# Performance work log

Measured on AMD Instinct MI355X. Metric: run time of the kernel, lower is better.

The kernel has to match this reference:

```python
import jax, jax.numpy as jnp
import numpy as np

NODE_DIM = 256
EDGE_DIM = 64
NUM_HEADS = 8
HEAD_DIM = NODE_DIM // NUM_HEADS
B, N = 2, 512


def setup_inputs() -> dict:
    key = jax.random.key(0)
    ks = jax.random.split(key, 16)
    s_n = 1.0 / np.sqrt(NODE_DIM)
    s_e = 1.0 / np.sqrt(EDGE_DIM)
    inp = {
        "node_tensors": jax.random.normal(ks[0], (B, N, NODE_DIM), jnp.float32),
        "edge_tensors": jax.random.normal(ks[1], (B, N, N, EDGE_DIM), jnp.float32),
        # nn.Linear params: W is [out, in], y = x @ W.T + b
        "Wnq": jax.random.uniform(ks[2], (NODE_DIM, NODE_DIM), jnp.float32, -s_n, s_n),
        "bnq": jax.random.uniform(ks[3], (NODE_DIM,), jnp.float32, -s_n, s_n),
        "Wnk": jax.random.uniform(ks[4], (NODE_DIM, NODE_DIM), jnp.float32, -s_n, s_n),
        "bnk": jax.random.uniform(ks[5], (NODE_DIM,), jnp.float32, -s_n, s_n),
        "Wnv": jax.random.uniform(ks[6], (NODE_DIM, NODE_DIM), jnp.float32, -s_n, s_n),
        "bnv": jax.random.uniform(ks[7], (NODE_DIM,), jnp.float32, -s_n, s_n),
        "Weq": jax.random.uniform(ks[8], (NODE_DIM, EDGE_DIM), jnp.float32, -s_e, s_e),
        "beq": jax.random.uniform(ks[9], (NODE_DIM,), jnp.float32, -s_e, s_e),
        "Wek": jax.random.uniform(ks[10], (NODE_DIM, EDGE_DIM), jnp.float32, -s_e, s_e),
        "bek": jax.random.uniform(ks[11], (NODE_DIM,), jnp.float32, -s_e, s_e),
        "Wev": jax.random.uniform(ks[12], (NODE_DIM, EDGE_DIM), jnp.float32, -s_e, s_e),
        "bev": jax.random.uniform(ks[13], (NODE_DIM,), jnp.float32, -s_e, s_e),
    }
    return inp


def _node_heads(x):
    # [B, N, node_dim] -> [B, H, N, Dh]
    b, n, _ = x.shape
    return x.reshape(b, n, NUM_HEADS, HEAD_DIM).transpose(0, 2, 1, 3)


def _edge_heads(x):
    # [B, N, N, node_dim] -> [B, H, N, N, Dh]
    b, n, m, _ = x.shape
    return x.reshape(b, n, m, NUM_HEADS, HEAD_DIM).transpose(0, 3, 1, 2, 4)


def reference(node_tensors, edge_tensors, Wnq, bnq, Wnk, bnk, Wnv, bnv,
              Weq, beq, Wek, bek, Wev, bev):
    scale = 1.0 / np.sqrt(HEAD_DIM)
    nq = _node_heads(node_tensors @ Wnq.T + bnq)  # [B,H,N,Dh]
    nk = _node_heads(node_tensors @ Wnk.T + bnk)
    nv = _node_heads(node_tensors @ Wnv.T + bnv)
    eq = _edge_heads(edge_tensors @ Weq.T + beq)  # [B,H,N,N,Dh]
    ek = _edge_heads(edge_tensors @ Wek.T + bek)
    ev = _edge_heads(edge_tensors @ Wev.T + bev)
    # qk[b,h,i,j] = sum_d (eq[bhijd] + nq[bhid]) * (ek[bhijd] + nk[bhjd])
    qk = (jnp.einsum('bhijd,bhijd->bhij', eq, ek)
          + jnp.einsum('bhijd,bhjd->bhij', eq, nk)
          + jnp.einsum('bhid,bhijd->bhij', nq, ek)
          + jnp.einsum('bhid,bhjd->bhij', nq, nk))
    att = jax.nn.softmax(qk * scale, axis=-1)  # [B,H,N,N]
    # out[b,h,i,d] = sum_j att[bhij] * (ev[bhijd] + nv[bhjd])
    out = (jnp.einsum('bhij,bhijd->bhid', att, ev)
           + jnp.einsum('bhij,bhjd->bhid', att, nv))
    b, h, n, d = out.shape
    return out.transpose(0, 2, 1, 3).reshape(b, n, NODE_DIM)
```

## Files before the change

### kernel.cpp

```cpp
#include <hip/hip_runtime.h>

typedef __bf16 bf16x8 __attribute__((ext_vector_type(8)));
typedef float  f32x4  __attribute__((ext_vector_type(4)));
typedef unsigned int u32x4 __attribute__((ext_vector_type(4)));

#define B_   2
#define N_   512
#define ND_  256
#define ED_  64
#define NH_  8
#define DH_  32

static __device__ __forceinline__ unsigned pack_bf16(float a, float b) {
    unsigned short ua = __builtin_bit_cast(unsigned short, (__bf16)a);
    unsigned short ub = __builtin_bit_cast(unsigned short, (__bf16)b);
    return (unsigned)ua | ((unsigned)ub << 16);
}

__global__ __launch_bounds__(256) void cvt_w_kernel(
    const float* __restrict__ wq, const float* __restrict__ wk,
    const float* __restrict__ wv, unsigned short* __restrict__ w16)
{
    int id = blockIdx.x * 256 + threadIdx.x;
    const float* src = (id < 16384) ? wq : (id < 32768 ? wk : wv);
    int idx = id & 16383;
    w16[id] = __builtin_bit_cast(unsigned short, (__bf16)src[idx]);
}

__global__ __launch_bounds__(256) void trans_w_kernel(
    const float* __restrict__ Wq, const float* __restrict__ Wk,
    const float* __restrict__ Wv, float* __restrict__ Wt)
{
    __shared__ float t[32][33];
    const int bx = blockIdx.x;
    const int m  = bx >> 6;
    const int t6 = bx & 63;
    const int cb = (t6 >> 3) << 5;
    const int kb = (t6 & 7) << 5;
    const float* W = (m == 0) ? Wq : (m == 1 ? Wk : Wv);
    const int tx = threadIdx.x & 31, ty = threadIdx.x >> 5;
    #pragma unroll
    for (int s = 0; s < 4; s++)
        t[ty + 8 * s][tx] = W[(size_t)(cb + ty + 8 * s) * ND_ + kb + tx];
    __syncthreads();
    float* dst = Wt + (size_t)m * ND_ * ND_;
    #pragma unroll
    for (int s = 0; s < 4; s++)
        dst[(size_t)(kb + ty + 8 * s) * ND_ + cb + tx] = t[tx][ty + 8 * s];
}

__global__ __launch_bounds__(256) void qkv_kernel(
    const float* __restrict__ node, const float* __restrict__ Wt,
    const float* __restrict__ bnq, const float* __restrict__ bnk,
    const float* __restrict__ bnv, const float* __restrict__ beq,
    const float* __restrict__ bek, const float* __restrict__ bev,
    float* __restrict__ Qh, float* __restrict__ KVp)
{
    __shared__ float xs[4][ND_];
    const int c   = threadIdx.x;
    const int m   = blockIdx.x >> 8;
    const int grp = blockIdx.x & 255;
    const int g0  = grp * 4;
    {
        const int r = c >> 6, col4 = (c & 63) * 4;
        const float4 v = *reinterpret_cast<const float4*>(node + (size_t)(g0 + r) * ND_ + col4);
        *reinterpret_cast<float4*>(&xs[r][col4]) = v;
    }
    __syncthreads();

    const float* Wm = Wt + (size_t)m * ND_ * ND_;
    float acc[4] = {0.f, 0.f, 0.f, 0.f};
    for (int k = 0; k < ND_; k += 4) {
        const float w0 = Wm[(size_t)(k + 0) * ND_ + c];
        const float w1 = Wm[(size_t)(k + 1) * ND_ + c];
        const float w2 = Wm[(size_t)(k + 2) * ND_ + c];
        const float w3 = Wm[(size_t)(k + 3) * ND_ + c];
        #pragma unroll
        for (int rr = 0; rr < 4; rr++) {
            const float4 x = *reinterpret_cast<const float4*>(&xs[rr][k]);
            acc[rr] += x.x * w0 + x.y * w1 + x.z * w2 + x.w * w3;
        }
    }
    const float bias = (m == 0) ? (bnq[c] + beq[c])
                     : (m == 1) ? (bnk[c] + bek[c])
                                : (bnv[c] + bev[c]);
    const int h = c >> 5, d = c & 31;
    #pragma unroll
    for (int rr = 0; rr < 4; rr++) {
        const int g  = g0 + rr;
        const int bb = g >> 9, ii = g & (N_ - 1);
        const int bh = bb * NH_ + h;
        const float y = acc[rr] + bias;
        if (m == 0) {
            Qh[((size_t)bh * N_ + ii) * DH_ + d] = y;
        } else {
            const int set = ((m == 1) ? 0 : 2) + (d >> 4);
            const size_t idx = (((size_t)bh * 32 + (ii >> 4)) * 4 + set) * 256
                             + (size_t)((((d >> 2) & 3) * 16 + (ii & 15)) * 4 + (d & 3));
            KVp[idx] = y;
        }
    }
}

__global__ __launch_bounds__(512, 2) void attn_kernel(
    const float* __restrict__ edge,
    const float* __restrict__ Qh, const float* __restrict__ KVp,
    const unsigned short* __restrict__ W16, float* __restrict__ out)
{
    __shared__ unsigned short lds_[2][2][64 * 72];

    const int tid  = threadIdx.x;
    const int lane = tid & 63;
    const int h    = tid >> 6;
    const int q4   = lane >> 4;
    const int l15  = lane & 15;
    const int blk  = blockIdx.x;
    const int b    = blk >> 8;
    const int i0   = (blk & 255) * 2;
    const int bh   = b * NH_ + h;

    bf16x8 wf[3][2][2];
    #pragma unroll
    for (int m = 0; m < 3; m++)
        #pragma unroll
        for (int hf = 0; hf < 2; hf++)
            #pragma unroll
            for (int ks = 0; ks < 2; ks++) {
                const u32x4* p = reinterpret_cast<const u32x4*>(
                    W16 + m * (ND_ * ED_) + (h * DH_ + hf * 16 + l15) * ED_ + ks * 32 + q4 * 8);
                wf[m][hf][ks] = __builtin_bit_cast(bf16x8, *p);
            }

    f32x4 Cq[2][2];
    {
        const float* Qrow = Qh + ((size_t)bh * N_ + i0) * DH_;
        Cq[0][0] = *reinterpret_cast<const f32x4*>(Qrow + q4 * 4);
        Cq[0][1] = *reinterpret_cast<const f32x4*>(Qrow + 16 + q4 * 4);
        Cq[1][0] = *reinterpret_cast<const f32x4*>(Qrow + DH_ + q4 * 4);
        Cq[1][1] = *reinterpret_cast<const f32x4*>(Qrow + DH_ + 16 + q4 * 4);
    }

    const f32x4* kvb = reinterpret_cast<const f32x4*>(KVp + (size_t)bh * 32 * 1024) + lane;

    const float* eb0 = edge + ((size_t)(b * N_ + i0)) * N_ * ED_;
    const float* eb1 = eb0 + (size_t)N_ * ED_;

    float l_acc[2] = {0.f, 0.f};
    f32x4 o0[2] = {{0.f,0.f,0.f,0.f},{0.f,0.f,0.f,0.f}};
    f32x4 o1[2] = {{0.f,0.f,0.f,0.f},{0.f,0.f,0.f,0.f}};
    const float scale = 0.17677669529663687f;

    float4 g[2][2];
    {
        const float4* e0 = reinterpret_cast<const float4*>(eb0);
        const float4* e1 = reinterpret_cast<const float4*>(eb1);
        g[0][0] = e0[tid]; g[0][1] = e0[tid + 512];
        g[1][0] = e1[tid]; g[1][1] = e1[tid + 512];
    }
    #pragma unroll
    for (int ii = 0; ii < 2; ii++) {
        unsigned short* buf = lds_[0][ii];
        #pragma unroll
        for (int pt = 0; pt < 2; pt++) {
            const float4 gg = g[ii][pt];
            const int f = tid + pt * 512;
            const int row = f >> 4, c4 = f & 15;
            uint2 v = {pack_bf16(gg.x, gg.y), pack_bf16(gg.z, gg.w)};
            *reinterpret_cast<uint2*>(buf + row * 72 + c4 * 4) = v;
        }
    }
    f32x4 kn0 = kvb[0], kn1 = kvb[64], vn0 = kvb[128], vn1 = kvb[192];
    __syncthreads();

    #pragma unroll 1
    for (int ch = 0; ch < 8; ch++) {
        if (ch < 7) {
            const float4* e0 = reinterpret_cast<const float4*>(eb0 + (ch + 1) * 4096);
            const float4* e1 = reinterpret_cast<const float4*>(eb1 + (ch + 1) * 4096);
            g[0][0] = e0[tid]; g[0][1] = e0[tid + 512];
            g[1][0] = e1[tid]; g[1][1] = e1[tid + 512];
        }
        const unsigned short* buf0 = lds_[ch & 1][0];
        const unsigned short* buf1 = lds_[ch & 1][1];

        #pragma unroll 2
        for (int sub = 0; sub < 4; sub++) {
            const int jg = ch * 4 + sub;
            const f32x4 Ck0 = kn0, Ck1 = kn1, Cv0 = vn0, Cv1 = vn1;
            {
                const f32x4* p = kvb + ((jg + 1) & 31) * 256;
                kn0 = p[0]; kn1 = p[64]; vn0 = p[128]; vn1 = p[192];
            }
            const unsigned short* ar0 = buf0 + (sub * 16 + l15) * 72 + q4 * 8;
            const unsigned short* ar1 = buf1 + (sub * 16 + l15) * 72 + q4 * 8;
            const bf16x8 a00 = __builtin_bit_cast(bf16x8, *reinterpret_cast<const u32x4*>(ar0));
            const bf16x8 a01 = __builtin_bit_cast(bf16x8, *reinterpret_cast<const u32x4*>(ar0 + 32));
            const bf16x8 a10 = __builtin_bit_cast(bf16x8, *reinterpret_cast<const u32x4*>(ar1));
            const bf16x8 a11 = __builtin_bit_cast(bf16x8, *reinterpret_cast<const u32x4*>(ar1 + 32));

            #pragma unroll
            for (int ii = 0; ii < 2; ii++) {
                const bf16x8 aA = ii ? a10 : a00;
                const bf16x8 aB = ii ? a11 : a01;
                f32x4 eq0 = __builtin_amdgcn_mfma_f32_16x16x32_bf16(wf[0][0][0], aA, Cq[ii][0], 0, 0, 0);
                f32x4 eq1 = __builtin_amdgcn_mfma_f32_16x16x32_bf16(wf[0][1][0], aA, Cq[ii][1], 0, 0, 0);
                f32x4 ek0 = __builtin_amdgcn_mfma_f32_16x16x32_bf16(wf[1][0][0], aA, Ck0, 0, 0, 0);
                f32x4 ek1 = __builtin_amdgcn_mfma_f32_16x16x32_bf16(wf[1][1][0], aA, Ck1, 0, 0, 0);
                f32x4 ev0 = __builtin_amdgcn_mfma_f32_16x16x32_bf16(wf[2][0][0], aA, Cv0, 0, 0, 0);
                f32x4 ev1 = __builtin_amdgcn_mfma_f32_16x16x32_bf16(wf[2][1][0], aA, Cv1, 0, 0, 0);
                eq0 = __builtin_amdgcn_mfma_f32_16x16x32_bf16(wf[0][0][1], aB, eq0, 0, 0, 0);
                eq1 = __builtin_amdgcn_mfma_f32_16x16x32_bf16(wf[0][1][1], aB, eq1, 0, 0, 0);
                ek0 = __builtin_amdgcn_mfma_f32_16x16x32_bf16(wf[1][0][1], aB, ek0, 0, 0, 0);
                ek1 = __builtin_amdgcn_mfma_f32_16x16x32_bf16(wf[1][1][1], aB, ek1, 0, 0, 0);
                ev0 = __builtin_amdgcn_mfma_f32_16x16x32_bf16(wf[2][0][1], aB, ev0, 0, 0, 0);
                ev1 = __builtin_amdgcn_mfma_f32_16x16x32_bf16(wf[2][1][1], aB, ev1, 0, 0, 0);

                float ta = eq0[0]*ek0[0] + eq0[1]*ek0[1];
                float tb = eq0[2]*ek0[2] + eq0[3]*ek0[3];
                float tc = eq1[0]*ek1[0] + eq1[1]*ek1[1];
                float td = eq1[2]*ek1[2] + eq1[3]*ek1[3];
                float t = (ta + tb) + (tc + td);
                t += __shfl_xor(t, 16, 64);
                t += __shfl_xor(t, 32, 64);
                const float p = __expf(fmaf(t, scale, -4.f));

                l_acc[ii] += p;
                o0[ii] += ev0 * p;
                o1[ii] += ev1 * p;
            }
        }

        if (ch < 7) {
            #pragma unroll
            for (int ii = 0; ii < 2; ii++) {
                unsigned short* nbuf = lds_[(ch + 1) & 1][ii];
                #pragma unroll
                for (int pt = 0; pt < 2; pt++) {
                    const float4 gg = g[ii][pt];
                    const int f = tid + pt * 512;
                    const int row = f >> 4, c4 = f & 15;
                    uint2 v = {pack_bf16(gg.x, gg.y), pack_bf16(gg.z, gg.w)};
                    *reinterpret_cast<uint2*>(nbuf + row * 72 + c4 * 4) = v;
                }
            }
        }
        __syncthreads();
    }

    #pragma unroll
    for (int mask = 1; mask <= 8; mask <<= 1) {
        #pragma unroll
        for (int ii = 0; ii < 2; ii++) {
            l_acc[ii] += __shfl_xor(l_acc[ii], mask, 64);
            #pragma unroll
            for (int r = 0; r < 4; r++) {
                o0[ii][r] += __shfl_xor(o0[ii][r], mask, 64);
                o1[ii][r] += __shfl_xor(o1[ii][r], mask, 64);
            }
        }
    }
    if (l15 == 0) {
        #pragma unroll
        for (int ii = 0; ii < 2; ii++) {
            const float inv = 1.f / l_acc[ii];
            float* orow = out + ((size_t)(b * N_ + i0 + ii)) * ND_ + h * DH_ + q4 * 4;
            float4 va = {o0[ii][0] * inv, o0[ii][1] * inv, o0[ii][2] * inv, o0[ii][3] * inv};
            float4 vb = {o1[ii][0] * inv, o1[ii][1] * inv, o1[ii][2] * inv, o1[ii][3] * inv};
            *reinterpret_cast<float4*>(orow)      = va;
            *reinterpret_cast<float4*>(orow + 16) = vb;
        }
    }
}

extern "C" void kernel_launch(void* const* d_in, const int* in_sizes, int n_in,
                              void* d_out, int out_size, void* d_ws, size_t ws_size,
                              hipStream_t stream) {
    const float* node = (const float*)d_in[0];
    const float* edge = (const float*)d_in[1];
    const float* Wnq  = (const float*)d_in[2];
    const float* bnq  = (const float*)d_in[3];
    const float* Wnk  = (const float*)d_in[4];
    const float* bnk  = (const float*)d_in[5];
    const float* Wnv  = (const float*)d_in[6];
    const float* bnv  = (const float*)d_in[7];
    const float* Weq  = (const float*)d_in[8];
    const float* beq  = (const float*)d_in[9];
    const float* Wek  = (const float*)d_in[10];
    const float* bek  = (const float*)d_in[11];
    const float* Wev  = (const float*)d_in[12];
    const float* bev  = (const float*)d_in[13];

    char* ws = (char*)d_ws;
    unsigned short* W16 = (unsigned short*)ws;
    float* Wt  = (float*)(ws + 131072);
    float* Qh  = (float*)(ws + 131072 + 786432);
    float* KVp = (float*)(ws + 131072 + 786432 + 1048576);
    float* out = (float*)d_out;

    cvt_w_kernel<<<192, 256, 0, stream>>>(Weq, Wek, Wev, W16);
    trans_w_kernel<<<192, 256, 0, stream>>>(Wnq, Wnk, Wnv, Wt);
    qkv_kernel<<<768, 256, 0, stream>>>(node, Wt, bnq, bnk, bnv, beq, bek, bev, Qh, KVp);
    attn_kernel<<<512, 512, 0, stream>>>(edge, Qh, KVp, W16, out);
}
```

Measured before the change: 272.7 us.

## Process four query rows per block with split-half edge prefetch pipeline

Each attention block now handles four query rows instead of two, so each K/V fragment load is reused across more rows, and the grid is halved to 256 blocks. Edge chunk loading is split into two halves whose global loads and LDS writes are interleaved between sub-steps. K/V prefetch is now two steps ahead, and s_setprio is raised around the MFMA bursts. The cost is more registers and LDS per block, and only 256 blocks, which may underfill the GPU's compute units and reduce latency hiding.

```diff
diff --git a/kernel.cpp b/kernel.cpp
--- a/kernel.cpp
+++ b/kernel.cpp
@@ -107,7 +107,7 @@
     const float* __restrict__ Qh, const float* __restrict__ KVp,
     const unsigned short* __restrict__ W16, float* __restrict__ out)
 {
-    __shared__ unsigned short lds_[2][2][64 * 72];
+    __shared__ unsigned short lds_[2][4][64 * 72];
 
     const int tid  = threadIdx.x;
     const int lane = tid & 63;
@@ -115,8 +115,8 @@
     const int q4   = lane >> 4;
     const int l15  = lane & 15;
     const int blk  = blockIdx.x;
-    const int b    = blk >> 8;
-    const int i0   = (blk & 255) * 2;
+    const int b    = blk >> 7;
+    const int i0   = (blk & 127) * 4;
     const int bh   = b * NH_ + h;
 
     bf16x8 wf[3][2][2];
@@ -131,126 +131,122 @@
                 wf[m][hf][ks] = __builtin_bit_cast(bf16x8, *p);
             }
 
-    f32x4 Cq[2][2];
+    f32x4 Cq[4][2];
     {
         const float* Qrow = Qh + ((size_t)bh * N_ + i0) * DH_;
-        Cq[0][0] = *reinterpret_cast<const f32x4*>(Qrow + q4 * 4);
-        Cq[0][1] = *reinterpret_cast<const f32x4*>(Qrow + 16 + q4 * 4);
-        Cq[1][0] = *reinterpret_cast<const f32x4*>(Qrow + DH_ + q4 * 4);
-        Cq[1][1] = *reinterpret_cast<const f32x4*>(Qrow + DH_ + 16 + q4 * 4);
+        #pragma unroll
+        for (int ii = 0; ii < 4; ii++) {
+            Cq[ii][0] = *reinterpret_cast<const f32x4*>(Qrow + ii * DH_ + q4 * 4);
+            Cq[ii][1] = *reinterpret_cast<const f32x4*>(Qrow + ii * DH_ + 16 + q4 * 4);
+        }
     }
 
     const f32x4* kvb = reinterpret_cast<const f32x4*>(KVp + (size_t)bh * 32 * 1024) + lane;
 
-    const float* eb0 = edge + ((size_t)(b * N_ + i0)) * N_ * ED_;
-    const float* eb1 = eb0 + (size_t)N_ * ED_;
-
-    float l_acc[2] = {0.f, 0.f};
-    f32x4 o0[2] = {{0.f,0.f,0.f,0.f},{0.f,0.f,0.f,0.f}};
-    f32x4 o1[2] = {{0.f,0.f,0.f,0.f},{0.f,0.f,0.f,0.f}};
+    const float* eb[4];
+    #pragma unroll
+    for (int ii = 0; ii < 4; ii++)
+        eb[ii] = edge + (size_t)(b * N_ + i0 + ii) * N_ * ED_;
+
+    float l_acc[4] = {0.f, 0.f, 0.f, 0.f};
+    f32x4 o0[4], o1[4];
+    #pragma unroll
+    for (int ii = 0; ii < 4; ii++) { o0[ii] = (f32x4){0.f,0.f,0.f,0.f}; o1[ii] = (f32x4){0.f,0.f,0.f,0.f}; }
     const float scale = 0.17677669529663687f;
 
-    float4 g[2][2];
-    {
-        const float4* e0 = reinterpret_cast<const float4*>(eb0);
-        const float4* e1 = reinterpret_cast<const float4*>(eb1);
-        g[0][0] = e0[tid]; g[0][1] = e0[tid + 512];
-        g[1][0] = e1[tid]; g[1][1] = e1[tid + 512];
-    }
-    #pragma unroll
-    for (int ii = 0; ii < 2; ii++) {
-        unsigned short* buf = lds_[0][ii];
-        #pragma unroll
-        for (int pt = 0; pt < 2; pt++) {
-            const float4 gg = g[ii][pt];
-            const int f = tid + pt * 512;
-            const int row = f >> 4, c4 = f & 15;
-            uint2 v = {pack_bf16(gg.x, gg.y), pack_bf16(gg.z, gg.w)};
-            *reinterpret_cast<uint2*>(buf + row * 72 + c4 * 4) = v;
-        }
-    }
-    f32x4 kn0 = kvb[0], kn1 = kvb[64], vn0 = kvb[128], vn1 = kvb[192];
+#define KV_PREFETCH(KA0, KA1, VA0, VA1, JG) do {                               \
+        const f32x4* pp_ = kvb + (size_t)((JG) & 31) * 256;                    \
+        KA0 = pp_[0]; KA1 = pp_[64]; VA0 = pp_[128]; VA1 = pp_[192];           \
+    } while (0)
+
+#define ISSUE_HALF(gA, gB, gC, gD, H, CN) do {                                 \
+        const float4* p0_ = reinterpret_cast<const float4*>(eb[(H)*2]     + (CN) * 4096); \
+        const float4* p1_ = reinterpret_cast<const float4*>(eb[(H)*2 + 1] + (CN) * 4096); \
+        gA = p0_[tid]; gB = p0_[tid + 512]; gC = p1_[tid]; gD = p1_[tid + 512]; \
+    } while (0)
+
+#define WRITE_HALF(gA, gB, gC, gD, H, NB) do {                                 \
+        unsigned short* b0_ = &lds_[NB][(H)*2][0];                             \
+        unsigned short* b1_ = &lds_[NB][(H)*2 + 1][0];                         \
+        { uint2 v_ = {pack_bf16(gA.x, gA.y), pack_bf16(gA.z, gA.w)};           \
+          *reinterpret_cast<uint2*>(b0_ + (tid >> 4) * 72 + (tid & 15) * 4) = v_; } \
+        { const int f_ = tid + 512;                                            \
+          uint2 v_ = {pack_bf16(gB.x, gB.y), pack_bf16(gB.z, gB.w)};           \
+          *reinterpret_cast<uint2*>(b0_ + (f_ >> 4) * 72 + (f_ & 15) * 4) = v_; } \
+        { uint2 v_ = {pack_bf16(gC.x, gC.y), pack_bf16(gC.z, gC.w)};           \
+          *reinterpret_cast<uint2*>(b1_ + (tid >> 4) * 72 + (tid & 15) * 4) = v_; } \
+        { const int f_ = tid + 512;                                            \
+          uint2 v_ = {pack_bf16(gD.x, gD.y), pack_bf16(gD.z, gD.w)};           \
+          *reinterpret_cast<uint2*>(b1_ + (f_ >> 4) * 72 + (f_ & 15) * 4) = v_; } \
+    } while (0)
+
+#define DO_SUB(SI, KA0, KA1, VA0, VA1) do {                                    \
+        const f32x4 Ck0 = KA0, Ck1 = KA1, Cv0 = VA0, Cv1 = VA1;                \
+        KV_PREFETCH(KA0, KA1, VA0, VA1, ch * 4 + (SI) + 2);                    \
+        const unsigned short* cbase_ = &lds_[ch & 1][0][0];                    \
+        _Pragma("unroll")                                                      \
+        for (int ii = 0; ii < 4; ii++) {                                       \
+            const unsigned short* ar_ = cbase_ + ii * (64 * 72)                \
+                                      + ((SI) * 16 + l15) * 72 + q4 * 8;       \
+            const bf16x8 aA = __builtin_bit_cast(bf16x8, *reinterpret_cast<const u32x4*>(ar_));      \
+            const bf16x8 aB = __builtin_bit_cast(bf16x8, *reinterpret_cast<const u32x4*>(ar_ + 32)); \
+            __builtin_amdgcn_s_setprio(1);                                     \
+            f32x4 eq0 = __builtin_amdgcn_mfma_f32_16x16x32_bf16(wf[0][0][0], aA, Cq[ii][0], 0, 0, 0); \
+            f32x4 eq1 = __builtin_amdgcn_mfma_f32_16x16x32_bf16(wf[0][1][0], aA, Cq[ii][1], 0, 0, 0); \
+            f32x4 ek0 = __builtin_amdgcn_mfma_f32_16x16x32_bf16(wf[1][0][0], aA, Ck0, 0, 0, 0);       \
+            f32x4 ek1 = __builtin_amdgcn_mfma_f32_16x16x32_bf16(wf[1][1][0], aA, Ck1, 0, 0, 0);       \
+            f32x4 ev0 = __builtin_amdgcn_mfma_f32_16x16x32_bf16(wf[2][0][0], aA, Cv0, 0, 0, 0);       \
+            f32x4 ev1 = __builtin_amdgcn_mfma_f32_16x16x32_bf16(wf[2][1][0], aA, Cv1, 0, 0, 0);       \
+            eq0 = __builtin_amdgcn_mfma_f32_16x16x32_bf16(wf[0][0][1], aB, eq0, 0, 0, 0);             \
+            eq1 = __builtin_amdgcn_mfma_f32_16x16x32_bf16(wf[0][1][1], aB, eq1, 0, 0, 0);             \
+            ek0 = __builtin_amdgcn_mfma_f32_16x16x32_bf16(wf[1][0][1], aB, ek0, 0, 0, 0);             \
+            ek1 = __builtin_amdgcn_mfma_f32_16x16x32_bf16(wf[1][1][1], aB, ek1, 0, 0, 0);             \
+            ev0 = __builtin_amdgcn_mfma_f32_16x16x32_bf16(wf[2][0][1], aB, ev0, 0, 0, 0);             \
+            ev1 = __builtin_amdgcn_mfma_f32_16x16x32_bf16(wf[2][1][1], aB, ev1, 0, 0, 0);             \
+            __builtin_amdgcn_s_setprio(0);                                     \
+            float ta = eq0[0]*ek0[0] + eq0[1]*ek0[1];                          \
+            float tb = eq0[2]*ek0[2] + eq0[3]*ek0[3];                          \
+            float tc = eq1[0]*ek1[0] + eq1[1]*ek1[1];                          \
+            float td = eq1[2]*ek1[2] + eq1[3]*ek1[3];                          \
+            float t = (ta + tb) + (tc + td);                                   \
+            t += __shfl_xor(t, 16, 64);                                        \
+            t += __shfl_xor(t, 32, 64);                                        \
+            const float p = __expf(fmaf(t, scale, -4.f));                      \
+            l_acc[ii] += p;                                                    \
+            o0[ii] += ev0 * p;                                                 \
+            o1[ii] += ev1 * p;                                                 \
+        }                                                                      \
+    } while (0)
+
+    float4 ga0, ga1, ga2, ga3, gb0, gb1, gb2, gb3;
+    ISSUE_HALF(ga0, ga1, ga2, ga3, 0, 0);
+    ISSUE_HALF(gb0, gb1, gb2, gb3, 1, 0);
+    WRITE_HALF(ga0, ga1, ga2, ga3, 0, 0);
+    WRITE_HALF(gb0, gb1, gb2, gb3, 1, 0);
+    f32x4 k0a, k0b, v0a, v0b, k1a, k1b, v1a, v1b;
+    KV_PREFETCH(k0a, k0b, v0a, v0b, 0);
+    KV_PREFETCH(k1a, k1b, v1a, v1b, 1);
     __syncthreads();
 
     #pragma unroll 1
     for (int ch = 0; ch < 8; ch++) {
+        if (ch < 7) ISSUE_HALF(ga0, ga1, ga2, ga3, 0, ch + 1);
+        DO_SUB(0, k0a, k0b, v0a, v0b);
+        DO_SUB(1, k1a, k1b, v1a, v1b);
         if (ch < 7) {
-            const float4* e0 = reinterpret_cast<const float4*>(eb0 + (ch + 1) * 4096);
-            const float4* e1 = reinterpret_cast<const float4*>(eb1 + (ch + 1) * 4096);
-            g[0][0] = e0[tid]; g[0][1] = e0[tid + 512];
-            g[1][0] = e1[tid]; g[1][1] = e1[tid + 512];
-        }
-        const unsigned short* buf0 = lds_[ch & 1][0];
-        const unsigned short* buf1 = lds_[ch & 1][1];
-
-        #pragma unroll 2
-        for (int sub = 0; sub < 4; sub++) {
-            const int jg = ch * 4 + sub;
-            const f32x4 Ck0 = kn0, Ck1 = kn1, Cv0 = vn0, Cv1 = vn1;
-            {
-                const f32x4* p = kvb + ((jg + 1) & 31) * 256;
-                kn0 = p[0]; kn1 = p[64]; vn0 = p[128]; vn1 = p[192];
-            }
-            const unsigned short* ar0 = buf0 + (sub * 16 + l15) * 72 + q4 * 8;
-            const unsigned short* ar1 = buf1 + (sub * 16 + l15) * 72 + q4 * 8;
-            const bf16x8 a00 = __builtin_bit_cast(bf16x8, *reinterpret_cast<const u32x4*>(ar0));
-            const bf16x8 a01 = __builtin_bit_cast(bf16x8, *reinterpret_cast<const u32x4*>(ar0 + 32));
-            const bf16x8 a10 = __builtin_bit_cast(bf16x8, *reinterpret_cast<const u32x4*>(ar1));
-            const bf16x8 a11 = __builtin_bit_cast(bf16x8, *reinterpret_cast<const u32x4*>(ar1 + 32));
-
-            #pragma unroll
-            for (int ii = 0; ii < 2; ii++) {
-                const bf16x8 aA = ii ? a10 : a00;
-                const bf16x8 aB = ii ? a11 : a01;
-                f32x4 eq0 = __builtin_amdgcn_mfma_f32_16x16x32_bf16(wf[0][0][0], aA, Cq[ii][0], 0, 0, 0);
-                f32x4 eq1 = __builtin_amdgcn_mfma_f32_16x16x32_bf16(wf[0][1][0], aA, Cq[ii][1], 0, 0, 0);
-                f32x4 ek0 = __builtin_amdgcn_mfma_f32_16x16x32_bf16(wf[1][0][0], aA, Ck0, 0, 0, 0);
-                f32x4 ek1 = __builtin_amdgcn_mfma_f32_16x16x32_bf16(wf[1][1][0], aA, Ck1, 0, 0, 0);
-                f32x4 ev0 = __builtin_amdgcn_mfma_f32_16x16x32_bf16(wf[2][0][0], aA, Cv0, 0, 0, 0);
-                f32x4 ev1 = __builtin_amdgcn_mfma_f32_16x16x32_bf16(wf[2][1][0], aA, Cv1, 0, 0, 0);
-                eq0 = __builtin_amdgcn_mfma_f32_16x16x32_bf16(wf[0][0][1], aB, eq0, 0, 0, 0);
-                eq1 = __builtin_amdgcn_mfma_f32_16x16x32_bf16(wf[0][1][1], aB, eq1, 0, 0, 0);
-                ek0 = __builtin_amdgcn_mfma_f32_16x16x32_bf16(wf[1][0][1], aB, ek0, 0, 0, 0);
-                ek1 = __builtin_amdgcn_mfma_f32_16x16x32_bf16(wf[1][1][1], aB, ek1, 0, 0, 0);
-                ev0 = __builtin_amdgcn_mfma_f32_16x16x32_bf16(wf[2][0][1], aB, ev0, 0, 0, 0);
-                ev1 = __builtin_amdgcn_mfma_f32_16x16x32_bf16(wf[2][1][1], aB, ev1, 0, 0, 0);
-
-                float ta = eq0[0]*ek0[0] + eq0[1]*ek0[1];
-                float tb = eq0[2]*ek0[2] + eq0[3]*ek0[3];
-                float tc = eq1[0]*ek1[0] + eq1[1]*ek1[1];
-                float td = eq1[2]*ek1[2] + eq1[3]*ek1[3];
-                float t = (ta + tb) + (tc + td);
-                t += __shfl_xor(t, 16, 64);
-                t += __shfl_xor(t, 32, 64);
-                const float p = __expf(fmaf(t, scale, -4.f));
-
-                l_acc[ii] += p;
-                o0[ii] += ev0 * p;
-                o1[ii] += ev1 * p;
-            }
-        }
-
-        if (ch < 7) {
-            #pragma unroll
-            for (int ii = 0; ii < 2; ii++) {
-                unsigned short* nbuf = lds_[(ch + 1) & 1][ii];
-                #pragma unroll
-                for (int pt = 0; pt < 2; pt++) {
-                    const float4 gg = g[ii][pt];
-                    const int f = tid + pt * 512;
-                    const int row = f >> 4, c4 = f & 15;
-                    uint2 v = {pack_bf16(gg.x, gg.y), pack_bf16(gg.z, gg.w)};
-                    *reinterpret_cast<uint2*>(nbuf + row * 72 + c4 * 4) = v;
-                }
-            }
-        }
+            WRITE_HALF(ga0, ga1, ga2, ga3, 0, (ch + 1) & 1);
+            ISSUE_HALF(gb0, gb1, gb2, gb3, 1, ch + 1);
+        }
+        DO_SUB(2, k0a, k0b, v0a, v0b);
+        DO_SUB(3, k1a, k1b, v1a, v1b);
+        if (ch < 7) WRITE_HALF(gb0, gb1, gb2, gb3, 1, (ch + 1) & 1);
         __syncthreads();
     }
 
     #pragma unroll
     for (int mask = 1; mask <= 8; mask <<= 1) {
         #pragma unroll
-        for (int ii = 0; ii < 2; ii++) {
+        for (int ii = 0; ii < 4; ii++) {
             l_acc[ii] += __shfl_xor(l_acc[ii], mask, 64);
             #pragma unroll
             for (int r = 0; r < 4; r++) {
@@ -261,7 +257,7 @@
     }
     if (l15 == 0) {
         #pragma unroll
-        for (int ii = 0; ii < 2; ii++) {
+        for (int ii = 0; ii < 4; ii++) {
             const float inv = 1.f / l_acc[ii];
             float* orow = out + ((size_t)(b * N_ + i0 + ii)) * ND_ + h * DH_ + q4 * 4;
             float4 va = {o0[ii][0] * inv, o0[ii][1] * inv, o0[ii][2] * inv, o0[ii][3] * inv};
@@ -270,6 +266,10 @@
             *reinterpret_cast<float4*>(orow + 16) = vb;
         }
     }
+#undef KV_PREFETCH
+#undef ISSUE_HALF
+#undef WRITE_HALF
+#undef DO_SUB
 }
 
 extern "C" void kernel_launch(void* const* d_in, const int* in_sizes, int n_in,
@@ -300,5 +300,5 @@
     cvt_w_kernel<<<192, 256, 0, stream>>>(Weq, Wek, Wev, W16);
     trans_w_kernel<<<192, 256, 0, stream>>>(Wnq, Wnk, Wnv, Wt);
     qkv_kernel<<<768, 256, 0, stream>>>(node, Wt, bnq, bnk, bnv, beq, bek, bev, Qh, KVp);
-    attn_kernel<<<512, 512, 0, stream>>>(edge, Qh, KVp, W16, out);
-}
+    attn_kernel<<<256, 512, 0, stream>>>(edge, Qh, KVp, W16, out);
+}
```

Measured after the change: 466.4 us. 71.0% more time.
